# Kernel tuning notes

Hardware: AMD Instinct MI355X
Metric: run time of the kernel (lower is better)

Reference implementation:

```python
import jax, jax.numpy as jnp
import numpy as np

B, N, DM, S = 128, 1024, 64, 2
D_IN = 1 + 1 + 2 + DM  # x(1) + m(1) + u(2) + h(DM)


def setup_inputs() -> dict:
    key = jax.random.key(0)
    ks = jax.random.split(key, 12)
    return {
        "x": jax.random.normal(ks[0], (B, 1, N), jnp.float32),
        "m": jax.random.uniform(ks[1], (B, 1, N), jnp.float32),
        "u": jax.random.normal(ks[2], (B, 2, N), jnp.float32),
        "h": jax.random.normal(ks[3], (B, DM, N), jnp.float32),
        # stack of support_len row-normalized-ish adjacencies [S, N, N]
        "adj": jax.random.uniform(ks[4], (S, N, N), jnp.float32) / N,
        "W_in": jax.random.normal(ks[5], (DM, D_IN), jnp.float32) * 0.05,
        "b_in": jnp.zeros((DM,), jnp.float32),
        "W_gc": jax.random.normal(ks[6], (DM, S * DM), jnp.float32) * 0.05,
        "b_gc": jnp.zeros((DM,), jnp.float32),
        "W_out": jax.random.normal(ks[7], (DM, 2 * DM), jnp.float32) * 0.05,
        "b_out": jnp.zeros((DM,), jnp.float32),
        "W_read": jax.random.normal(ks[8], (1, 2 * DM), jnp.float32) * 0.05,
        "b_read": jnp.zeros((1,), jnp.float32),
        "prelu_w": jnp.full((1,), 0.25, jnp.float32),
    }


def _conv1x1(x, W, b):
    # Conv1d(kernel_size=1): [b,c,n] x [o,c] -> [b,o,n]
    return jnp.einsum('bcn,oc->bon', x, W) + b[None, :, None]


def reference(x, m, u, h, adj, W_in, b_in, W_gc, b_gc, W_out, b_out, W_read, b_read, prelu_w):
    # concat inputs on channel dim, then 1x1 conv to d_model
    x_in = jnp.concatenate([x, m, u, h], axis=1)            # [b, d_in, n]
    x_in = _conv1x1(x_in, W_in, b_in)                        # [b, dm, n]
    # SpatialConvOrderK (order=1, include_self=False):
    # per-support aggregation einsum('ncvl,wv->ncwl') with l==1
    agg = jnp.einsum('bcv,swv->bscw', x_in, adj)             # [b, S, dm, n]
    b_, s_, c_, n_ = agg.shape
    agg = agg.reshape(b_, s_ * c_, n_)                       # support-major concat
    gc = _conv1x1(agg, W_gc, b_gc)                           # [b, dm, n]
    out = jnp.concatenate([gc, h], axis=1)                   # [b, 2dm, n]
    out = _conv1x1(out, W_out, b_out)
    out = jnp.where(out >= 0, out, prelu_w[0] * out)         # PReLU (1 param)
    out = jnp.concatenate([out, h], axis=1)                  # [b, 2dm, n]
    return _conv1x1(out, W_read, b_read), out
```

## Files before the change

kernel.cpp:

```cpp
#include <hip/hip_runtime.h>
#include <hip/hip_bf16.h>
#include <stdint.h>

#define NB 128
#define NN 1024
#define NDM 64

typedef __bf16 bf16;
typedef __bf16 bf16x8_t __attribute__((ext_vector_type(8)));
typedef __bf16 bf16x4_t __attribute__((ext_vector_type(4)));
typedef float f32x4 __attribute__((ext_vector_type(4)));

__global__ __launch_bounds__(256) void k_prep(
    const float* __restrict__ adj,
    const float* __restrict__ W_in, const float* __restrict__ b_in,
    const float* __restrict__ W_gc, const float* __restrict__ b_gc,
    const float* __restrict__ W_out, const float* __restrict__ b_out,
    const float* __restrict__ W_read,
    bf16* __restrict__ adjb, bf16* __restrict__ WAT, float* __restrict__ WYX,
    float* __restrict__ BIAS, bf16* __restrict__ W1B, bf16* __restrict__ A2B,
    float* __restrict__ HBv) {
  const int bx = blockIdx.x;
  if (bx < 2048) {
    int i = bx * 256 + threadIdx.x;
    float4 v = reinterpret_cast<const float4*>(adj)[i];
    bf16x4_t r;
    r.x = (bf16)v.x; r.y = (bf16)v.y; r.z = (bf16)v.z; r.w = (bf16)v.w;
    reinterpret_cast<bf16x4_t*>(adjb)[i] = r;
    return;
  }
  int i = (bx - 2048) * 256 + threadIdx.x;
  if (i < 8192) {
    int r = i >> 6, cc = i & 63;
    int cq = cc >> 3, j = cc & 7;
    int c = ((cq ^ (r & 7)) << 3) + j;
    int s = r >> 6, o = r & 63;
    float val = 0.f;
    for (int k = 0; k < 64; ++k) val += W_gc[o * 128 + s * 64 + k] * W_in[k * 68 + 4 + c];
    WAT[i] = (bf16)val;
  } else if (i < 8704) {
    int idx = i - 8192;
    int r = idx >> 2, jj = idx & 3;
    int s = r >> 6, o = r & 63;
    float val = 0.f;
    for (int k = 0; k < 64; ++k) val += W_gc[o * 128 + s * 64 + k] * W_in[k * 68 + jj];
    WYX[idx] = val;
  } else if (i < 8832) {
    int r = i - 8704;
    int s = r >> 6, o = r & 63;
    float val = 0.f;
    for (int k = 0; k < 64; ++k) val += W_gc[o * 128 + s * 64 + k] * b_in[k];
    BIAS[r] = val;
  } else if (i < 12928) {
    int j = i - 8832;
    int o = j >> 6, c = j & 63;
    W1B[j] = (bf16)W_out[o * 128 + c];
  } else if (i < 18048) {
    int j = i - 12928;
    int r = j >> 6, c = j & 63;
    float val = 0.f;
    if (r < 64) val = W_out[r * 128 + 64 + c];
    else if (r == 64) val = W_read[64 + c];
    A2B[j] = (bf16)val;
  } else if (i < 18112) {
    int o = i - 18048;
    float val = b_out[o];
    for (int c = 0; c < 64; ++c) val += W_out[o * 128 + c] * b_gc[c];
    HBv[o] = val;
  }
}

__global__ __launch_bounds__(256) void k_build(
    const float* __restrict__ x, const float* __restrict__ m, const float* __restrict__ u,
    const float* __restrict__ h, const bf16* __restrict__ WAT,
    const float* __restrict__ WYX, const float* __restrict__ BIAS,
    bf16* __restrict__ Y, bf16* __restrict__ HT, float* __restrict__ out2) {
  __shared__ __align__(16) float T[64 * 128];
  __shared__ __align__(16) bf16 HTs[128 * 64];
  __shared__ __align__(16) bf16 WAs[128 * 64];
  __shared__ __align__(16) float X4L[128 * 4];
  __shared__ __align__(16) float WYXs[128 * 4];
  __shared__ __align__(16) float biasL[128];
  const int t = threadIdx.x;
  const int vb = blockIdx.x * 128;
  const int b = blockIdx.y;

  for (int i = t; i < 2048; i += 256)
    __builtin_amdgcn_global_load_lds(
        (const uint32_t*)(h + (size_t)(b * 64 + (i >> 5)) * NN + vb + (i & 31) * 4),
        (uint32_t*)&T[i * 4], 16, 0, 0);
  for (int i = t; i < 1024; i += 256)
    __builtin_amdgcn_global_load_lds((const uint32_t*)(WAT + i * 8), (uint32_t*)&WAs[i * 8], 16, 0, 0);
  if (t < 128)
    __builtin_amdgcn_global_load_lds((const uint32_t*)(WYX + t * 4), (uint32_t*)&WYXs[t * 4], 16, 0, 0);
  if (t < 32)
    __builtin_amdgcn_global_load_lds((const uint32_t*)(BIAS + t * 4), (uint32_t*)&biasL[t * 4], 16, 0, 0);
  if (t < 128) {
    float4 x4;
    x4.x = x[(size_t)b * NN + vb + t];
    x4.y = m[(size_t)b * NN + vb + t];
    x4.z = u[(size_t)(b * 2) * NN + vb + t];
    x4.w = u[(size_t)(b * 2 + 1) * NN + vb + t];
    *reinterpret_cast<float4*>(&X4L[t * 4]) = x4;
  }
  __syncthreads();

  {
    const int v = t >> 1, half = t & 1;
#pragma unroll
    for (int cc = 0; cc < 4; ++cc) {
      int cq = half * 4 + cc;
      int cbase = (cq ^ (v & 7)) << 3;
      bf16x8_t pk;
#pragma unroll
      for (int j = 0; j < 8; ++j) pk[j] = (bf16)T[(cbase + j) * 128 + v];
      *reinterpret_cast<bf16x8_t*>(&HTs[v * 64 + cq * 8]) = pk;
      *reinterpret_cast<bf16x8_t*>(&HT[((size_t)(b << 10) + vb + v) * 64 + cq * 8]) = pk;
    }
  }
  for (int i = t; i < 2048; i += 256) {
    int r = i >> 5, ck = i & 31;
    float4 hv = *reinterpret_cast<const float4*>(&T[r * 128 + ck * 4]);
    *reinterpret_cast<float4*>(&out2[(size_t)(b * 128 + 64 + r) * NN + vb + ck * 4]) = hv;
  }
  __syncthreads();

  const int wave = t >> 6, lane = t & 63;
  const int q = lane >> 4, lx = lane & 7, o16 = lane & 15;
  const int offK0 = (q ^ lx) << 3, offK1 = ((q + 4) ^ lx) << 3;

#pragma unroll
  for (int vi = 0; vi < 2; ++vi) {
    const int vt = wave + vi * 4;
    const int vrow = vt * 16 + o16;
    bf16x8_t af0 = *reinterpret_cast<const bf16x8_t*>(&HTs[vrow * 64 + offK0]);
    bf16x8_t af1 = *reinterpret_cast<const bf16x8_t*>(&HTs[vrow * 64 + offK1]);
    float4 x4r[4];
#pragma unroll
    for (int r = 0; r < 4; ++r)
      x4r[r] = *reinterpret_cast<const float4*>(&X4L[(vt * 16 + q * 4 + r) * 4]);
    const int vg = vb + vt * 16 + q * 4;
    for (int nt = 0; nt < 8; ++nt) {
      const int rr = nt * 16 + o16;
      bf16x8_t bf0 = *reinterpret_cast<const bf16x8_t*>(&WAs[rr * 64 + offK0]);
      bf16x8_t bf1 = *reinterpret_cast<const bf16x8_t*>(&WAs[rr * 64 + offK1]);
      float bsv = biasL[rr];
      float4 wy = *reinterpret_cast<const float4*>(&WYXs[rr * 4]);
      f32x4 c0;
#pragma unroll
      for (int r = 0; r < 4; ++r)
        c0[r] = bsv + wy.x * x4r[r].x + wy.y * x4r[r].y + wy.z * x4r[r].z + wy.w * x4r[r].w;
      f32x4 acc = __builtin_amdgcn_mfma_f32_16x16x32_bf16(af0, bf0, c0, 0, 0, 0);
      acc = __builtin_amdgcn_mfma_f32_16x16x32_bf16(af1, bf1, acc, 0, 0, 0);
      const int s = nt >> 2;
      const int o = rr - s * 64;
      bf16x4_t pk;
      pk.x = (bf16)acc[0]; pk.y = (bf16)acc[1]; pk.z = (bf16)acc[2]; pk.w = (bf16)acc[3];
      *reinterpret_cast<bf16x4_t*>(&Y[(size_t)(b * 64 + o) * 2048 + s * 1024 + vg]) = pk;
    }
  }
}

__global__ __launch_bounds__(512, 2) void k_gemm(
    const bf16* __restrict__ Y, const bf16* __restrict__ ADJB,
    const bf16* __restrict__ HT,
    const bf16* __restrict__ W1B, const bf16* __restrict__ A2B,
    const float* __restrict__ HBv, const float* __restrict__ W_read,
    const float* __restrict__ b_read, const float* __restrict__ prelu_w,
    float* __restrict__ out0, float* __restrict__ out2) {
  __shared__ __align__(16) union SMem {
    struct { bf16 As[2][256 * 64]; bf16 Bs[2][128 * 64]; } st;
    bf16 gcs[4 * 128 * 72];
  } sm;
  __shared__ __align__(16) bf16 W1s[64 * 72];
  __shared__ __align__(16) bf16 A2s[80 * 72];
  __shared__ float HBs[64];
  __shared__ float Wrs[64];

  const int t = threadIdx.x;
  const int wave = t >> 6, lane = t & 63;
  const int lin = blockIdx.y * 32 + blockIdx.x;
  const int xcd = lin & 7, rest = lin >> 3;
  const int rowA = (xcd * 4 + (rest >> 3)) * 256;
  const int colB = (rest & 7) * 128;
  const int wm = (wave >> 1) * 64, wn = (wave & 1) * 64;
  const int fr = lane & 15;
  const int q = lane >> 4, lx = lane & 7;
  const int offK0 = (q ^ lx) << 3, offK1 = ((q + 4) ^ lx) << 3;

  {
    const int r = t >> 3, c8 = t & 7;
    *reinterpret_cast<bf16x8_t*>(&W1s[r * 72 + c8 * 8]) =
        *reinterpret_cast<const bf16x8_t*>(&W1B[t * 8]);
  }
  for (int i = t; i < 640; i += 512) {
    const int r = i >> 3, c8 = i & 7;
    *reinterpret_cast<bf16x8_t*>(&A2s[r * 72 + c8 * 8]) =
        *reinterpret_cast<const bf16x8_t*>(&A2B[i * 8]);
  }
  if (t < 64) { HBs[t] = HBv[t]; Wrs[t] = W_read[t]; }
  const float pw = prelu_w[0];
  const float br = b_read[0];

  f32x4 acc[4][4];
  const f32x4 zero = {0.f, 0.f, 0.f, 0.f};
#pragma unroll
  for (int i = 0; i < 4; ++i)
#pragma unroll
    for (int j = 0; j < 4; ++j) acc[i][j] = zero;

  auto stage = [&](int d, int kt) {
    const int kg = kt * 64;
    const int s = kg >> 10, v0 = kg & 1023;
#pragma unroll
    for (int ja = 0; ja < 4; ++ja) {
      const int c = t + 512 * ja;
      const int row = c >> 3;
      const int qs = ((c & 7) ^ (row & 7)) << 3;
      __builtin_amdgcn_global_load_lds(
          (const uint32_t*)(Y + (size_t)(rowA + row) * 2048 + kg + qs),
          (uint32_t*)&sm.st.As[d][c * 8], 16, 0, 0);
    }
#pragma unroll
    for (int jb = 0; jb < 2; ++jb) {
      const int c = t + 512 * jb;
      const int row = c >> 3;
      const int qs = ((c & 7) ^ (row & 7)) << 3;
      __builtin_amdgcn_global_load_lds(
          (const uint32_t*)(ADJB + ((size_t)s << 20) + (size_t)(colB + row) * 1024 + v0 + qs),
          (uint32_t*)&sm.st.Bs[d][c * 8], 16, 0, 0);
    }
  };

  int rAb[4], rBb[4];
#pragma unroll
  for (int i = 0; i < 4; ++i) {
    rAb[i] = (wm + i * 16 + fr) * 64;
    rBb[i] = (wn + i * 16 + fr) * 64;
  }

  stage(0, 0);
  stage(1, 1);

#pragma unroll 2
  for (int kt = 0; kt < 32; ++kt) {
    const int cur = kt & 1;
    if (kt < 31) asm volatile("s_waitcnt vmcnt(6)" ::: "memory");
    else         asm volatile("s_waitcnt vmcnt(0)" ::: "memory");
    __builtin_amdgcn_s_barrier();
    const bf16* A_ = sm.st.As[cur];
    const bf16* B_ = sm.st.Bs[cur];
    bf16x8_t af0[4], bf0[4], af1[4], bf1[4];
#pragma unroll
    for (int i = 0; i < 4; ++i) af0[i] = *reinterpret_cast<const bf16x8_t*>(&A_[rAb[i] + offK0]);
#pragma unroll
    for (int i = 0; i < 4; ++i) bf0[i] = *reinterpret_cast<const bf16x8_t*>(&B_[rBb[i] + offK0]);
    asm volatile("s_waitcnt lgkmcnt(0)" ::: "memory");
    __builtin_amdgcn_sched_barrier(0);
    __builtin_amdgcn_s_setprio(1);
#pragma unroll
    for (int i = 0; i < 4; ++i)
#pragma unroll
      for (int j = 0; j < 4; ++j)
        acc[i][j] = __builtin_amdgcn_mfma_f32_16x16x32_bf16(af0[i], bf0[j], acc[i][j], 0, 0, 0);
    __builtin_amdgcn_s_setprio(0);
#pragma unroll
    for (int i = 0; i < 4; ++i) af1[i] = *reinterpret_cast<const bf16x8_t*>(&A_[rAb[i] + offK1]);
#pragma unroll
    for (int i = 0; i < 4; ++i) bf1[i] = *reinterpret_cast<const bf16x8_t*>(&B_[rBb[i] + offK1]);
    asm volatile("s_waitcnt lgkmcnt(0)" ::: "memory");
    __builtin_amdgcn_sched_barrier(0);
    __builtin_amdgcn_s_barrier();
    if (kt < 30) stage(cur, kt + 2);
    __builtin_amdgcn_s_setprio(1);
#pragma unroll
    for (int i = 0; i < 4; ++i)
#pragma unroll
      for (int j = 0; j < 4; ++j)
        acc[i][j] = __builtin_amdgcn_mfma_f32_16x16x32_bf16(af1[i], bf1[j], acc[i][j], 0, 0, 0);
    __builtin_amdgcn_s_setprio(0);
  }

  {
    const int b2w = wm >> 6;
#pragma unroll
    for (int i = 0; i < 4; ++i) {
      const int cc0 = i * 16 + q * 4;
#pragma unroll
      for (int j = 0; j < 4; ++j) {
        const int wl = wn + j * 16 + fr;
        bf16x4_t r;
        r.x = (bf16)acc[i][j][0]; r.y = (bf16)acc[i][j][1];
        r.z = (bf16)acc[i][j][2]; r.w = (bf16)acc[i][j][3];
        *reinterpret_cast<bf16x4_t*>(&sm.gcs[b2w * 9216 + wl * 72 + cc0]) = r;
      }
    }
  }
  __syncthreads();

  const int b2 = wave >> 1, jh = wave & 1;
  const int b = (rowA >> 6) + b2;

  f32x4 acc2[5][4];
#pragma unroll
  for (int i = 0; i < 5; ++i)
#pragma unroll
    for (int j = 0; j < 4; ++j) {
      if (i < 4) {
        f32x4 c0;
#pragma unroll
        for (int r = 0; r < 4; ++r) c0[r] = HBs[i * 16 + q * 4 + r];
        acc2[i][j] = c0;
      } else {
        acc2[i][j] = zero;
      }
    }

#pragma unroll
  for (int k2 = 0; k2 < 64; k2 += 32) {
    bf16x8_t af2[4], bf2[4];
#pragma unroll
    for (int i = 0; i < 4; ++i)
      af2[i] = *reinterpret_cast<const bf16x8_t*>(&W1s[(i * 16 + fr) * 72 + k2 + q * 8]);
#pragma unroll
    for (int j = 0; j < 4; ++j)
      bf2[j] = *reinterpret_cast<const bf16x8_t*>(&sm.gcs[b2 * 9216 + (jh * 64 + j * 16 + fr) * 72 + k2 + q * 8]);
#pragma unroll
    for (int i = 0; i < 4; ++i)
#pragma unroll
      for (int j = 0; j < 4; ++j)
        acc2[i][j] = __builtin_amdgcn_mfma_f32_16x16x32_bf16(af2[i], bf2[j], acc2[i][j], 0, 0, 0);
  }

#pragma unroll
  for (int k2 = 0; k2 < 64; k2 += 32) {
    const int off = k2 ? offK1 : offK0;
    bf16x8_t bh[4], af3[5];
#pragma unroll
    for (int j = 0; j < 4; ++j) {
      const int w = colB + jh * 64 + j * 16 + fr;
      bh[j] = *reinterpret_cast<const bf16x8_t*>(&HT[((size_t)(b << 10) + w) * 64 + off]);
    }
#pragma unroll
    for (int i = 0; i < 5; ++i)
      af3[i] = *reinterpret_cast<const bf16x8_t*>(&A2s[(i * 16 + fr) * 72 + k2 + q * 8]);
#pragma unroll
    for (int i = 0; i < 5; ++i)
#pragma unroll
      for (int j = 0; j < 4; ++j)
        acc2[i][j] = __builtin_amdgcn_mfma_f32_16x16x32_bf16(af3[i], bh[j], acc2[i][j], 0, 0, 0);
  }

  float rd[4] = {0.f, 0.f, 0.f, 0.f};
#pragma unroll
  for (int i = 0; i < 4; ++i) {
#pragma unroll
    for (int r = 0; r < 4; ++r) {
      const int o = i * 16 + q * 4 + r;
      const float wr = Wrs[o];
#pragma unroll
      for (int j = 0; j < 4; ++j) {
        const int wg = colB + jh * 64 + j * 16 + fr;
        float val = acc2[i][j][r];
        val = val >= 0.f ? val : pw * val;
        out2[(size_t)(b * 128 + o) * 1024 + wg] = val;
        rd[j] += wr * val;
      }
    }
  }
#pragma unroll
  for (int j = 0; j < 4; ++j) {
    rd[j] += __shfl_xor(rd[j], 16, 64);
    rd[j] += __shfl_xor(rd[j], 32, 64);
  }
  if (lane < 16) {
#pragma unroll
    for (int j = 0; j < 4; ++j) {
      const int wg = colB + jh * 64 + j * 16 + lane;
      out0[(size_t)b * 1024 + wg] = rd[j] + acc2[4][j][0] + br;
    }
  }
}

extern "C" void kernel_launch(void* const* d_in, const int* in_sizes, int n_in,
                              void* d_out, int out_size, void* d_ws, size_t ws_size,
                              hipStream_t stream) {
  (void)in_sizes; (void)n_in; (void)out_size; (void)ws_size;
  const float* x       = (const float*)d_in[0];
  const float* m       = (const float*)d_in[1];
  const float* u       = (const float*)d_in[2];
  const float* h       = (const float*)d_in[3];
  const float* adj     = (const float*)d_in[4];
  const float* W_in    = (const float*)d_in[5];
  const float* b_in    = (const float*)d_in[6];
  const float* W_gc    = (const float*)d_in[7];
  const float* b_gc    = (const float*)d_in[8];
  const float* W_out   = (const float*)d_in[9];
  const float* b_out   = (const float*)d_in[10];
  const float* W_read  = (const float*)d_in[11];
  const float* b_read  = (const float*)d_in[12];
  const float* prelu_w = (const float*)d_in[13];

  char* ws = (char*)d_ws;
  bf16*  Y    = (bf16*)(ws);
  bf16*  ADJB = (bf16*)(ws + 33554432);
  bf16*  HT   = (bf16*)(ws + 37748736);
  bf16*  WAT  = (bf16*)(ws + 54525952);
  float* WYX  = (float*)(ws + 54542336);
  float* BIAS = (float*)(ws + 54544384);
  bf16*  W1B  = (bf16*)(ws + 54544896);
  bf16*  A2B  = (bf16*)(ws + 54553088);
  float* HBv  = (float*)(ws + 54563328);

  float* out0 = (float*)d_out;
  float* out2 = out0 + 131072;

  hipLaunchKernelGGL(k_prep,  dim3(2119),     dim3(256), 0, stream,
                     adj, W_in, b_in, W_gc, b_gc, W_out, b_out, W_read,
                     ADJB, WAT, WYX, BIAS, W1B, A2B, HBv);
  hipLaunchKernelGGL(k_build, dim3(8, 128),   dim3(256), 0, stream,
                     x, m, u, h, WAT, WYX, BIAS, Y, HT, out2);
  hipLaunchKernelGGL(k_gemm,  dim3(32, 8),    dim3(512), 0, stream,
                     Y, ADJB, HT, W1B, A2B, HBv, W_read, b_read, prelu_w, out0, out2);
}
```

Baseline: 182.6 us.

## Triple-buffer GEMM main loop and overlay epilogue smem onto stage buffers

Raises the global-to-LDS prefetch depth in the main aggregation GEMM from two to three stages, replacing per-stage address math with incrementing source pointers. All LDS fragment reads for an iteration are now issued before the first MFMA batch, with a partial lgkmcnt wait, to overlap LDS latency with compute. Epilogue weights and scratch are moved into a union with the stage buffers and loaded after the loop, so the extra buffer fits in shared memory. Shared memory use rises from about 98 KB to about 144 KB, which with 512-thread blocks and launch_bounds(512,2) likely cuts residency from 2 blocks per CU to 1.

```diff
diff --git a/kernel.cpp b/kernel.cpp
--- a/kernel.cpp
+++ b/kernel.cpp
@@ -169,13 +169,15 @@
     const float* __restrict__ b_read, const float* __restrict__ prelu_w,
     float* __restrict__ out0, float* __restrict__ out2) {
   __shared__ __align__(16) union SMem {
-    struct { bf16 As[2][256 * 64]; bf16 Bs[2][128 * 64]; } st;
-    bf16 gcs[4 * 128 * 72];
+    struct { bf16 As[3][256 * 64]; bf16 Bs[3][128 * 64]; } st;
+    struct {
+      bf16 gcs[4 * 128 * 72];
+      bf16 W1s[64 * 72];
+      bf16 A2s[80 * 72];
+      float HBs[64];
+      float Wrs[64];
+    } ep;
   } sm;
-  __shared__ __align__(16) bf16 W1s[64 * 72];
-  __shared__ __align__(16) bf16 A2s[80 * 72];
-  __shared__ float HBs[64];
-  __shared__ float Wrs[64];
 
   const int t = threadIdx.x;
   const int wave = t >> 6, lane = t & 63;
@@ -188,20 +190,6 @@
   const int q = lane >> 4, lx = lane & 7;
   const int offK0 = (q ^ lx) << 3, offK1 = ((q + 4) ^ lx) << 3;
 
-  {
-    const int r = t >> 3, c8 = t & 7;
-    *reinterpret_cast<bf16x8_t*>(&W1s[r * 72 + c8 * 8]) =
-        *reinterpret_cast<const bf16x8_t*>(&W1B[t * 8]);
-  }
-  for (int i = t; i < 640; i += 512) {
-    const int r = i >> 3, c8 = i & 7;
-    *reinterpret_cast<bf16x8_t*>(&A2s[r * 72 + c8 * 8]) =
-        *reinterpret_cast<const bf16x8_t*>(&A2B[i * 8]);
-  }
-  if (t < 64) { HBs[t] = HBv[t]; Wrs[t] = W_read[t]; }
-  const float pw = prelu_w[0];
-  const float br = b_read[0];
-
   f32x4 acc[4][4];
   const f32x4 zero = {0.f, 0.f, 0.f, 0.f};
 #pragma unroll
@@ -209,26 +197,34 @@
 #pragma unroll
     for (int j = 0; j < 4; ++j) acc[i][j] = zero;
 
-  auto stage = [&](int d, int kt) {
-    const int kg = kt * 64;
-    const int s = kg >> 10, v0 = kg & 1023;
+  const bf16* aSrc[4]; const bf16* bSrc[2];
+#pragma unroll
+  for (int j = 0; j < 4; ++j) {
+    const int c = t + 512 * j;
+    const int row = c >> 3;
+    const int qs = ((c & 7) ^ (row & 7)) << 3;
+    aSrc[j] = Y + (size_t)(rowA + row) * 2048 + qs;
+  }
+#pragma unroll
+  for (int j = 0; j < 2; ++j) {
+    const int c = t + 512 * j;
+    const int row = c >> 3;
+    const int qs = ((c & 7) ^ (row & 7)) << 3;
+    bSrc[j] = ADJB + (size_t)(colB + row) * 1024 + qs;
+  }
+
+  auto stage = [&](int d) {
 #pragma unroll
     for (int ja = 0; ja < 4; ++ja) {
-      const int c = t + 512 * ja;
-      const int row = c >> 3;
-      const int qs = ((c & 7) ^ (row & 7)) << 3;
-      __builtin_amdgcn_global_load_lds(
-          (const uint32_t*)(Y + (size_t)(rowA + row) * 2048 + kg + qs),
-          (uint32_t*)&sm.st.As[d][c * 8], 16, 0, 0);
+      __builtin_amdgcn_global_load_lds((const uint32_t*)aSrc[ja],
+                                       (uint32_t*)&sm.st.As[d][(t + 512 * ja) * 8], 16, 0, 0);
+      aSrc[ja] += 64;
     }
 #pragma unroll
     for (int jb = 0; jb < 2; ++jb) {
-      const int c = t + 512 * jb;
-      const int row = c >> 3;
-      const int qs = ((c & 7) ^ (row & 7)) << 3;
-      __builtin_amdgcn_global_load_lds(
-          (const uint32_t*)(ADJB + ((size_t)s << 20) + (size_t)(colB + row) * 1024 + v0 + qs),
-          (uint32_t*)&sm.st.Bs[d][c * 8], 16, 0, 0);
+      __builtin_amdgcn_global_load_lds((const uint32_t*)bSrc[jb],
+                                       (uint32_t*)&sm.st.Bs[d][(t + 512 * jb) * 8], 16, 0, 0);
+      bSrc[jb] += 64;
     }
   };
 
@@ -239,14 +235,13 @@
     rBb[i] = (wn + i * 16 + fr) * 64;
   }
 
-  stage(0, 0);
-  stage(1, 1);
-
-#pragma unroll 2
+  stage(0); stage(1); stage(2);
+
+  int cur = 0;
   for (int kt = 0; kt < 32; ++kt) {
-    const int cur = kt & 1;
-    if (kt < 31) asm volatile("s_waitcnt vmcnt(6)" ::: "memory");
-    else         asm volatile("s_waitcnt vmcnt(0)" ::: "memory");
+    if (kt < 30)       asm volatile("s_waitcnt vmcnt(12)" ::: "memory");
+    else if (kt == 30) asm volatile("s_waitcnt vmcnt(6)" ::: "memory");
+    else               asm volatile("s_waitcnt vmcnt(0)" ::: "memory");
     __builtin_amdgcn_s_barrier();
     const bf16* A_ = sm.st.As[cur];
     const bf16* B_ = sm.st.Bs[cur];
@@ -255,7 +250,12 @@
     for (int i = 0; i < 4; ++i) af0[i] = *reinterpret_cast<const bf16x8_t*>(&A_[rAb[i] + offK0]);
 #pragma unroll
     for (int i = 0; i < 4; ++i) bf0[i] = *reinterpret_cast<const bf16x8_t*>(&B_[rBb[i] + offK0]);
-    asm volatile("s_waitcnt lgkmcnt(0)" ::: "memory");
+    __builtin_amdgcn_sched_barrier(0);
+#pragma unroll
+    for (int i = 0; i < 4; ++i) af1[i] = *reinterpret_cast<const bf16x8_t*>(&A_[rAb[i] + offK1]);
+#pragma unroll
+    for (int i = 0; i < 4; ++i) bf1[i] = *reinterpret_cast<const bf16x8_t*>(&B_[rBb[i] + offK1]);
+    asm volatile("s_waitcnt lgkmcnt(8)" ::: "memory");
     __builtin_amdgcn_sched_barrier(0);
     __builtin_amdgcn_s_setprio(1);
 #pragma unroll
@@ -264,14 +264,16 @@
       for (int j = 0; j < 4; ++j)
         acc[i][j] = __builtin_amdgcn_mfma_f32_16x16x32_bf16(af0[i], bf0[j], acc[i][j], 0, 0, 0);
     __builtin_amdgcn_s_setprio(0);
-#pragma unroll
-    for (int i = 0; i < 4; ++i) af1[i] = *reinterpret_cast<const bf16x8_t*>(&A_[rAb[i] + offK1]);
-#pragma unroll
-    for (int i = 0; i < 4; ++i) bf1[i] = *reinterpret_cast<const bf16x8_t*>(&B_[rBb[i] + offK1]);
     asm volatile("s_waitcnt lgkmcnt(0)" ::: "memory");
     __builtin_amdgcn_sched_barrier(0);
     __builtin_amdgcn_s_barrier();
-    if (kt < 30) stage(cur, kt + 2);
+    if (kt < 29) {
+      stage(cur);
+      if (kt == 12) {
+        bSrc[0] += 1024 * 1024 - 1024;
+        bSrc[1] += 1024 * 1024 - 1024;
+      }
+    }
     __builtin_amdgcn_s_setprio(1);
 #pragma unroll
     for (int i = 0; i < 4; ++i)
@@ -279,7 +281,22 @@
       for (int j = 0; j < 4; ++j)
         acc[i][j] = __builtin_amdgcn_mfma_f32_16x16x32_bf16(af1[i], bf1[j], acc[i][j], 0, 0, 0);
     __builtin_amdgcn_s_setprio(0);
-  }
+    cur = (cur == 2) ? 0 : cur + 1;
+  }
+
+  {
+    const int r = t >> 3, c8 = t & 7;
+    *reinterpret_cast<bf16x8_t*>(&sm.ep.W1s[r * 72 + c8 * 8]) =
+        *reinterpret_cast<const bf16x8_t*>(&W1B[t * 8]);
+  }
+  for (int i = t; i < 640; i += 512) {
+    const int r = i >> 3, c8 = i & 7;
+    *reinterpret_cast<bf16x8_t*>(&sm.ep.A2s[r * 72 + c8 * 8]) =
+        *reinterpret_cast<const bf16x8_t*>(&A2B[i * 8]);
+  }
+  if (t < 64) { sm.ep.HBs[t] = HBv[t]; sm.ep.Wrs[t] = W_read[t]; }
+  const float pw = prelu_w[0];
+  const float br = b_read[0];
 
   {
     const int b2w = wm >> 6;
@@ -292,7 +309,7 @@
         bf16x4_t r;
         r.x = (bf16)acc[i][j][0]; r.y = (bf16)acc[i][j][1];
         r.z = (bf16)acc[i][j][2]; r.w = (bf16)acc[i][j][3];
-        *reinterpret_cast<bf16x4_t*>(&sm.gcs[b2w * 9216 + wl * 72 + cc0]) = r;
+        *reinterpret_cast<bf16x4_t*>(&sm.ep.gcs[b2w * 9216 + wl * 72 + cc0]) = r;
       }
     }
   }
@@ -309,7 +326,7 @@
       if (i < 4) {
         f32x4 c0;
 #pragma unroll
-        for (int r = 0; r < 4; ++r) c0[r] = HBs[i * 16 + q * 4 + r];
+        for (int r = 0; r < 4; ++r) c0[r] = sm.ep.HBs[i * 16 + q * 4 + r];
         acc2[i][j] = c0;
       } else {
         acc2[i][j] = zero;
@@ -321,10 +338,10 @@
     bf16x8_t af2[4], bf2[4];
 #pragma unroll
     for (int i = 0; i < 4; ++i)
-      af2[i] = *reinterpret_cast<const bf16x8_t*>(&W1s[(i * 16 + fr) * 72 + k2 + q * 8]);
+      af2[i] = *reinterpret_cast<const bf16x8_t*>(&sm.ep.W1s[(i * 16 + fr) * 72 + k2 + q * 8]);
 #pragma unroll
     for (int j = 0; j < 4; ++j)
-      bf2[j] = *reinterpret_cast<const bf16x8_t*>(&sm.gcs[b2 * 9216 + (jh * 64 + j * 16 + fr) * 72 + k2 + q * 8]);
+      bf2[j] = *reinterpret_cast<const bf16x8_t*>(&sm.ep.gcs[b2 * 9216 + (jh * 64 + j * 16 + fr) * 72 + k2 + q * 8]);
 #pragma unroll
     for (int i = 0; i < 4; ++i)
 #pragma unroll
@@ -343,7 +360,7 @@
     }
 #pragma unroll
     for (int i = 0; i < 5; ++i)
-      af3[i] = *reinterpret_cast<const bf16x8_t*>(&A2s[(i * 16 + fr) * 72 + k2 + q * 8]);
+      af3[i] = *reinterpret_cast<const bf16x8_t*>(&sm.ep.A2s[(i * 16 + fr) * 72 + k2 + q * 8]);
 #pragma unroll
     for (int i = 0; i < 5; ++i)
 #pragma unroll
@@ -357,7 +374,7 @@
 #pragma unroll
     for (int r = 0; r < 4; ++r) {
       const int o = i * 16 + q * 4 + r;
-      const float wr = Wrs[o];
+      const float wr = sm.ep.Wrs[o];
 #pragma unroll
       for (int j = 0; j < 4; ++j) {
         const int wg = colB + jh * 64 + j * 16 + fr;
```

New measurement: 182.4 us. No clear change (-0.1%).
